# Performance work log

Hardware: AMD Instinct MI355X
Metric: run time of the kernel (lower is better)

## Reference

```python
import jax, jax.numpy as jnp
import numpy as np

BOUNDARY_THRESHOLD = 0.5
TARGET_N = 6.0          # target_avg_token_length
RATIO_LOSS_WEIGHT = 0.03
LR_DIFF = 0.75          # learning_rate_difference
EPS = 1e-8              # torch cosine_similarity eps


def setup_inputs() -> dict:
    key = jax.random.key(0)
    k1, k2, k3 = jax.random.split(key, 3)
    B, L, D, DK = 8, 4096, 1024, 1024
    tokens = jax.random.normal(k1, (B, L, D), dtype=jnp.float32)
    W_qk = jax.random.normal(k2, (D, 2 * DK), dtype=jnp.float32) / np.sqrt(D).astype(np.float32)
    start_key = jax.random.normal(k3, (DK,), dtype=jnp.float32) * 0.01
    return {"tokens": tokens, "W_qk": W_qk, "start_key": start_key}


def _forward(tokens, W_qk, start_key):
    B, L, D = tokens.shape
    qk = tokens @ W_qk                                   # [B, L, 2*Dk]
    queries, keys = jnp.split(qk, 2, axis=-1)
    # keys shifted right by one, with learned start key prepended
    keys_for_sim = jnp.concatenate(
        [jnp.broadcast_to(start_key, (B, 1, keys.shape[-1])), keys[:, :-1]], axis=1)
    qn = jnp.maximum(jnp.linalg.norm(queries, axis=-1), EPS)
    kn = jnp.maximum(jnp.linalg.norm(keys_for_sim, axis=-1), EPS)
    cosine_sim = jnp.sum(queries * keys_for_sim, axis=-1) / (qn * kn)   # [B, L]
    probs = (1.0 - cosine_sim) * 0.5

    boundary_mask = probs > BOUNDARY_THRESHOLD
    boundary_mask = boundary_mask.at[:, 0].set(True)     # first step: first token is boundary
    num_chunks = jnp.sum(boundary_mask, axis=-1)         # [B]

    ar = jnp.arange(L)
    valid = ar[None, :] < num_chunks[:, None]            # [B, L] mask of valid (non-pad) chunks

    # chunk_lens via sorted boundary positions with end sentinel (pads -> length 0)
    bm_end = jnp.concatenate([boundary_mask, jnp.ones((B, 1), dtype=bool)], axis=1)  # [B, L+1]
    pos = jnp.sort(jnp.where(bm_end, jnp.arange(L + 1)[None, :], L + 1), axis=-1)
    chunk_lens = jnp.where(valid, pos[:, 1:] - pos[:, :-1], 0)          # [B, L]

    # compact boundary tokens / probs to the front (pad_sequence equivalent, padded to L)
    bpos = jnp.sort(jnp.where(boundary_mask, ar[None, :], L), axis=-1)  # [B, L]
    safe = jnp.minimum(bpos, L - 1)
    boundary_tokens = jnp.where(valid[..., None],
                                jnp.take_along_axis(tokens, safe[..., None], axis=1), 0.0)
    boundary_probs = jnp.where(valid, jnp.take_along_axis(probs, safe, axis=1), 0.0)
    downsampled = boundary_tokens * boundary_probs[..., None]

    # aux ratio loss (straight-through soft fraction)
    F_hard = boundary_mask.astype(probs.dtype)
    F_soft = jax.nn.sigmoid(probs - BOUNDARY_THRESHOLD)
    F = F_soft + jax.lax.stop_gradient(F_hard - F_soft)
    G = jnp.mean(probs, axis=-1)
    Fm = jnp.mean(F, axis=-1)
    N = TARGET_N
    aux_ratio_loss = N / (N - 1.0) * ((N - 1.0) * Fm * G + (1.0 - Fm) * (1.0 - G))
    weighted_aux_loss = jnp.mean(aux_ratio_loss) * RATIO_LOSS_WEIGHT

    # frac_gradient with frac = 1 / learning_rate_difference (identity fwd, scaled grad)
    frac = 1.0 / LR_DIFF
    ds_scaled = downsampled * frac
    downsampled = ds_scaled + jax.lax.stop_gradient(downsampled - ds_scaled)

    return downsampled, chunk_lens, weighted_aux_loss


def reference(tokens, W_qk, start_key):
    return _forward(tokens, W_qk, start_key)
```

## Files before the change

kernel.cpp:

```cpp
#include <hip/hip_runtime.h>
#include <hip/hip_bf16.h>
#include <hip/hip_fp16.h>


#define B_ 8
#define L_ 4096
#define D_ 1024
#define M_TOT (B_ * L_)
#define BM 128
#define DS_ELEMS ((size_t)M_TOT * D_)
#define SUS_CAP 2048

typedef _Float16 f16x8 __attribute__((ext_vector_type(8)));
typedef _Float16 f16x4 __attribute__((ext_vector_type(4)));
typedef __bf16  bf16x8 __attribute__((ext_vector_type(8)));
typedef __bf16  bf16x4 __attribute__((ext_vector_type(4)));
typedef float   f32x4  __attribute__((ext_vector_type(4)));

typedef __attribute__((address_space(1))) void gv_t;
typedef __attribute__((address_space(3))) void lv_t;

__device__ __forceinline__ void gl_lds16(const void* g, void* l) {
    __builtin_amdgcn_global_load_lds((gv_t*)g, (lv_t*)l, 16, 0, 0);
}

__global__ __launch_bounds__(256)
void prep(const float* __restrict__ tokens, const float* __restrict__ W,
          _Float16* __restrict__ t_h, _Float16* __restrict__ wT_h,
          __bf16* __restrict__ wT_hi, __bf16* __restrict__ wT_lo,
          float* __restrict__ zbase, float* __restrict__ aux_out)
{
    const int bid = blockIdx.x, tid = threadIdx.x;
    if (bid < 8192) {
        const size_t base = (size_t)bid * 4096 + tid * 4;
        #pragma unroll
        for (int r = 0; r < 4; ++r) {
            size_t idx = base + (size_t)r * 1024;
            float4 v = *(const float4*)&tokens[idx];
            f16x4 h;
            h[0] = (_Float16)v.x; h[1] = (_Float16)v.y;
            h[2] = (_Float16)v.z; h[3] = (_Float16)v.w;
            *(f16x4*)&t_h[idx] = h;
        }
    } else if (bid < 10240) {
        __shared__ float lw[32 * 33];
        const int local = bid - 8192;
        const int k0 = (local & 31) * 32;
        const int n0 = (local >> 5) * 32;
        {
            const int lk = tid >> 3, ln4 = (tid & 7) * 4;
            float4 v = *(const float4*)&W[(size_t)(k0 + lk) * 2048 + n0 + ln4];
            lw[(ln4 + 0) * 33 + lk] = v.x;
            lw[(ln4 + 1) * 33 + lk] = v.y;
            lw[(ln4 + 2) * 33 + lk] = v.z;
            lw[(ln4 + 3) * 33 + lk] = v.w;
        }
        __syncthreads();
        {
            const int ln = tid >> 3, lk4 = (tid & 7) * 4;
            f16x4 h; bf16x4 bh, bl;
            #pragma unroll
            for (int j = 0; j < 4; ++j) {
                float v = lw[ln * 33 + lk4 + j];
                h[j] = (_Float16)v;
                __bf16 b = (__bf16)v;
                bh[j] = b;
                bl[j] = (__bf16)(v - (float)b);
            }
            size_t o = (size_t)(n0 + ln) * 1024 + k0 + lk4;
            *(f16x4*)&wT_h[o]   = h;
            *(bf16x4*)&wT_hi[o] = bh;
            *(bf16x4*)&wT_lo[o] = bl;
        }
    } else {
        const int zb = bid - 10240;
        const int i = zb * 1024 + tid * 4;
        if (i < 98308)
            *(float4*)&zbase[i] = make_float4(0.f, 0.f, 0.f, 0.f);
        if (zb == 0 && tid == 0) *aux_out = 0.f;
    }
}

__global__ __launch_bounds__(512, 2)
void gemm_cos_f16(const _Float16* __restrict__ t_h, const _Float16* __restrict__ wT_h,
                  float* __restrict__ dotw, float* __restrict__ qn2w,
                  float* __restrict__ ksn2w,
                  float* __restrict__ qrow, float* __restrict__ krow)
{
    __shared__ float smem[33280];
    float* Ck = smem;

    const int bx = blockIdx.x;
    const int tile_n = (bx >> 3) & 7;
    const int tile_m = ((bx >> 6) & 15) + ((bx & 7) << 4);
    const int m0 = tile_m * 256;
    const int n0 = tile_n * 128;
    const int tid  = threadIdx.x;
    const int w    = tid >> 6;
    const int lane = tid & 63;
    const int quad = lane >> 4;
    const int lc   = lane & 15;

    const int wm  = (w & 3) * 64;
    const int wq0 = (w >> 2) * 64;

    const int st_ch = ((lane & 3) ^ ((lane >> 3) & 3)) * 8;
    const int ia0 = w * 2, ia1 = w * 2 + 1;
    const size_t a_g0 = (size_t)(m0 + ia0 * 16 + (lane >> 2)) * 1024 + st_ch;
    const size_t a_g1 = a_g0 + (size_t)16 * 1024;
    size_t b_g[2];
    #pragma unroll
    for (int j = 0; j < 2; ++j) {
        const int br = (w * 2 + j) * 16 + (lane >> 2);
        const int gr = (br < 128) ? (n0 + br) : (896 + n0 + br);
        b_g[j] = (size_t)gr * 1024 + st_ch;
    }

    char* const sb  = (char*)smem;
    char* const sbB = sb + 49152;
    const int fr_ch = (quad ^ ((lc >> 1) & 3)) * 8;

    f32x4 accq[4][4] = {};
    f32x4 acck[4][4] = {};

#define STAGE_A(KK, BASE)                                                    \
    {                                                                        \
        const size_t kb = (size_t)(KK) * 32;                                 \
        gl_lds16(t_h + a_g0 + kb, (BASE) + ia0 * 1024);                      \
        gl_lds16(t_h + a_g1 + kb, (BASE) + ia1 * 1024);                      \
    }
#define STAGE_B(KK, BASE)                                                    \
    {                                                                        \
        const size_t kb = (size_t)(KK) * 32;                                 \
        gl_lds16(wT_h + b_g[0] + kb, (BASE) + (w * 2 + 0) * 1024);           \
        gl_lds16(wT_h + b_g[1] + kb, (BASE) + (w * 2 + 1) * 1024);           \
    }

    STAGE_A(0, sb)
    STAGE_B(0, sbB)
    STAGE_A(1, sb + 16384)

    int acur = 0;
    int apre = 2;
    for (int kk = 0; kk < 32; ++kk) {
        if (kk < 31) {
            asm volatile("s_waitcnt vmcnt(2)" ::: "memory");
        } else {
            asm volatile("s_waitcnt vmcnt(0)" ::: "memory");
        }
        __builtin_amdgcn_s_barrier();
        if (kk < 31) STAGE_B(kk + 1, sbB + ((kk + 1) & 1) * 16384)
        if (kk < 30) STAGE_A(kk + 2, sb + apre * 16384)

        const _Float16* As = (const _Float16*)(sb + acur * 16384);
        const _Float16* Bs = (const _Float16*)(sbB + (kk & 1) * 16384);

        f16x8 af[4], bq[4], bk[4];
        #pragma unroll
        for (int mi = 0; mi < 4; ++mi)
            af[mi] = *(const f16x8*)(As + (wm + mi * 16 + lc) * 32 + fr_ch);
        #pragma unroll
        for (int ni = 0; ni < 4; ++ni) {
            bq[ni] = *(const f16x8*)(Bs + (wq0 + ni * 16 + lc) * 32 + fr_ch);
            bk[ni] = *(const f16x8*)(Bs + (128 + wq0 + ni * 16 + lc) * 32 + fr_ch);
        }
        #pragma unroll
        for (int mi = 0; mi < 4; ++mi) {
            #pragma unroll
            for (int ni = 0; ni < 4; ++ni) {
                accq[mi][ni] = __builtin_amdgcn_mfma_f32_16x16x32_f16(
                    af[mi], bq[ni], accq[mi][ni], 0, 0, 0);
                acck[mi][ni] = __builtin_amdgcn_mfma_f32_16x16x32_f16(
                    af[mi], bk[ni], acck[mi][ni], 0, 0, 0);
            }
        }
        acur = (acur == 2) ? 0 : acur + 1;
        apre = (apre == 2) ? 0 : apre + 1;
    }
#undef STAGE_A
#undef STAGE_B
    __syncthreads();

    #pragma unroll
    for (int mi = 0; mi < 4; ++mi) {
        #pragma unroll
        for (int reg = 0; reg < 4; ++reg) {
            const int row = wm + mi * 16 + quad * 4 + reg;
            float s = 0.f, s2 = 0.f;
            #pragma unroll
            for (int ni = 0; ni < 4; ++ni) {
                s  += accq[mi][ni][reg] * accq[mi][ni][reg];
                s2 += acck[mi][ni][reg] * acck[mi][ni][reg];
            }
            s += __shfl_xor(s, 1); s += __shfl_xor(s, 2);
            s += __shfl_xor(s, 4); s += __shfl_xor(s, 8);
            if (lc == 0) atomicAdd(&qn2w[m0 + row], s);

            s2 += __shfl_xor(s2, 1); s2 += __shfl_xor(s2, 2);
            s2 += __shfl_xor(s2, 4); s2 += __shfl_xor(s2, 8);
            if (lc == 0 && row < 255) atomicAdd(&ksn2w[m0 + row + 1], s2);
        }
    }

    #pragma unroll
    for (int mi = 0; mi < 4; ++mi)
        #pragma unroll
        for (int ni = 0; ni < 4; ++ni)
            #pragma unroll
            for (int reg = 0; reg < 4; ++reg)
                Ck[(wm + mi * 16 + quad * 4 + reg) * 130 + wq0 + ni * 16 + lc] =
                    acck[mi][ni][reg];
    __syncthreads();

    #pragma unroll
    for (int mi = 0; mi < 4; ++mi) {
        #pragma unroll
        for (int reg = 0; reg < 4; ++reg) {
            const int row = wm + mi * 16 + quad * 4 + reg;
            float d = 0.f;
            if (row >= 1) {
                #pragma unroll
                for (int ni = 0; ni < 4; ++ni)
                    d += accq[mi][ni][reg]
                       * Ck[(row - 1) * 130 + wq0 + ni * 16 + lc];
            }
            d += __shfl_xor(d, 1); d += __shfl_xor(d, 2);
            d += __shfl_xor(d, 4); d += __shfl_xor(d, 8);
            if (lc == 0 && row >= 1) atomicAdd(&dotw[m0 + row], d);
        }
    }

    if (wm == 0 && quad == 0) {
        #pragma unroll
        for (int ni = 0; ni < 4; ++ni)
            qrow[(size_t)(tile_m * 2) * D_ + n0 + wq0 + ni * 16 + lc] =
                accq[0][ni][0];
    }
    if (wm == 128 && quad == 0) {
        #pragma unroll
        for (int ni = 0; ni < 4; ++ni)
            qrow[(size_t)(tile_m * 2 + 1) * D_ + n0 + wq0 + ni * 16 + lc] =
                accq[0][ni][0];
    }
    if (wm == 64 && quad == 3) {
        #pragma unroll
        for (int ni = 0; ni < 4; ++ni)
            krow[(size_t)(tile_m * 2) * D_ + n0 + wq0 + ni * 16 + lc] =
                acck[3][ni][3];
    }
    if (wm == 192 && quad == 3) {
        #pragma unroll
        for (int ni = 0; ni < 4; ++ni)
            krow[(size_t)(tile_m * 2 + 1) * D_ + n0 + wq0 + ni * 16 + lc] =
                acck[3][ni][3];
    }
}

__global__ __launch_bounds__(256)
void probs_fused(const float* __restrict__ qrow, const float* __restrict__ krow,
                 const float* __restrict__ start_key,
                 const float* __restrict__ dotw, const float* __restrict__ qn2w,
                 const float* __restrict__ ksn2w, float* __restrict__ probsw,
                 int* __restrict__ scount, int* __restrict__ slist)
{
    const int tile = blockIdx.x;
    const int tid = threadIdx.x;
    __shared__ float sd[4], sk[4];

    {
        const float* q  = qrow + (size_t)tile * D_;
        const float* ks = ((tile & 31) == 0) ? start_key
                                             : (krow + (size_t)(tile - 1) * D_);
        float4 qv = *(const float4*)&q[tid * 4];
        float4 kv = *(const float4*)&ks[tid * 4];
        float d  = qv.x * kv.x + qv.y * kv.y + qv.z * kv.z + qv.w * kv.w;
        float k2 = kv.x * kv.x + kv.y * kv.y + kv.z * kv.z + kv.w * kv.w;
        #pragma unroll
        for (int off = 32; off; off >>= 1) {
            d  += __shfl_down(d, off, 64);
            k2 += __shfl_down(k2, off, 64);
        }
        const int lane = tid & 63, wid = tid >> 6;
        if (lane == 0) { sd[wid] = d; sk[wid] = k2; }
    }
    __syncthreads();

    if (tid < BM) {
        const int m = tile * BM + tid;
        float dd = dotw[m], kk = ksn2w[m];
        if (tid == 0) {
            dd = sd[0] + sd[1] + sd[2] + sd[3];
            kk = sk[0] + sk[1] + sk[2] + sk[3];
        }
        float qn = fmaxf(sqrtf(qn2w[m]), 1e-8f);
        float kn = fmaxf(sqrtf(kk), 1e-8f);
        float c = dd / (qn * kn);
        probsw[m] = 0.5f * (1.f - c);
        if (fabsf(c) < 1e-3f) {
            int i = atomicAdd(scount, 1);
            if (i < SUS_CAP) slist[i] = m;
        }
    }
}

__global__ __launch_bounds__(256)
void gather_split(const float* __restrict__ tokens, const int* __restrict__ scount,
                  const int* __restrict__ slist,
                  __bf16* __restrict__ As_hi, __bf16* __restrict__ As_lo)
{
    int n = *scount; if (n > SUS_CAP) n = SUS_CAP;
    const int n_up = (n + 127) & ~127;
    const int slot = blockIdx.x;
    const int sl = slot & 2047;
    if (sl >= n_up) return;
    const int tid = threadIdx.x;

    int src = -1;
    if (sl < n) {
        int t = slist[sl];
        if (slot < 2048) src = t;
        else src = ((t & 4095) == 0) ? t : (t - 1);
    }
    bf16x4 h = {}, l = {};
    if (src >= 0) {
        float4 v = *(const float4*)&tokens[(size_t)src * 1024 + tid * 4];
        float vs[4] = {v.x, v.y, v.z, v.w};
        #pragma unroll
        for (int j = 0; j < 4; ++j) {
            __bf16 b = (__bf16)vs[j];
            h[j] = b;
            l[j] = (__bf16)(vs[j] - (float)b);
        }
    }
    size_t o = (size_t)slot * 1024 + tid * 4;
    *(bf16x4*)&As_hi[o] = h;
    *(bf16x4*)&As_lo[o] = l;
}

__global__ __launch_bounds__(256, 2)
void gemm2(const __bf16* __restrict__ As_hi, const __bf16* __restrict__ As_lo,
           const __bf16* __restrict__ wT_hi, const __bf16* __restrict__ wT_lo,
           const int* __restrict__ scount, float* __restrict__ C2)
{
    int n = *scount; if (n > SUS_CAP) n = SUS_CAP;
    const int tm = blockIdx.y;
    const int local_base = (tm < 16) ? tm * 128 : (tm - 16) * 128;
    if (local_base >= n) return;
    const int m0 = (tm < 16) ? tm * 128 : 2048 + (tm - 16) * 128;

    __shared__ float smem[12288];

    const int tile_n = blockIdx.x;
    const int n0 = tile_n * 128;
    const int colbase = ((tm < 16) ? 0 : 1024) + n0;
    const int tid  = threadIdx.x;
    const int w    = tid >> 6;
    const int lane = tid & 63;
    const int quad = lane >> 4;
    const int lc   = lane & 15;
    const int wm  = (w & 1) * 64;
    const int wq0 = (w >> 1) * 32;

    const int ia0 = w * 2, ia1 = w * 2 + 1;
    const int st_ch = ((lane & 3) ^ ((lane >> 3) & 3)) * 8;
    const size_t a_g0 = (size_t)(m0 + ia0 * 16 + (lane >> 2)) * 1024 + st_ch;
    const size_t a_g1 = a_g0 + (size_t)16 * 1024;
    const int br0 = ia0 * 16 + (lane >> 2);
    const int br1 = br0 + 16;
    const size_t b_g0 = (size_t)(colbase + br0) * 1024 + st_ch;
    const size_t b_g1 = (size_t)(colbase + br1) * 1024 + st_ch;

    char* const sb = (char*)smem;
    const int fr_ch = (quad ^ ((lc >> 1) & 3)) * 8;

    f32x4 accq[4][2] = {};
    f32x4 acck[4][2] = {};

    gl_lds16(As_hi + a_g0,      sb + ia0 * 1024);
    gl_lds16(As_hi + a_g1,      sb + ia1 * 1024);
    gl_lds16(wT_hi + b_g0,      sb + 8192 + ia0 * 1024);
    gl_lds16(wT_hi + b_g1,      sb + 8192 + ia1 * 1024);
    gl_lds16(As_hi + a_g0 + 32, sb + 16384 + ia0 * 1024);
    gl_lds16(As_hi + a_g1 + 32, sb + 16384 + ia1 * 1024);
    gl_lds16(wT_hi + b_g0 + 32, sb + 16384 + 8192 + ia0 * 1024);
    gl_lds16(wT_hi + b_g1 + 32, sb + 16384 + 8192 + ia1 * 1024);

    int cur = 0;
    for (int kk = 0; kk < 96; ++kk) {
        if (kk < 95) {
            asm volatile("s_waitcnt vmcnt(4)" ::: "memory");
        } else {
            asm volatile("s_waitcnt vmcnt(0)" ::: "memory");
        }
        __builtin_amdgcn_s_barrier();
        if (kk < 94) {
            const int k2 = kk + 2;
            const int slab2 = k2 >> 5;
            const size_t kb2 = (size_t)(k2 & 31) * 32;
            const __bf16* Ap2 = (slab2 < 2) ? As_hi : As_lo;
            const __bf16* Bp2 = (slab2 == 1) ? wT_lo : wT_hi;
            int nxt = cur + 2; if (nxt >= 3) nxt -= 3;
            char* nb = sb + nxt * 16384;
            gl_lds16(Ap2 + a_g0 + kb2, nb + ia0 * 1024);
            gl_lds16(Ap2 + a_g1 + kb2, nb + ia1 * 1024);
            gl_lds16(Bp2 + b_g0 + kb2, nb + 8192 + ia0 * 1024);
            gl_lds16(Bp2 + b_g1 + kb2, nb + 8192 + ia1 * 1024);
        }
        const __bf16* As = (const __bf16*)(sb + cur * 16384);
        const __bf16* Bs = As + 4096;

        bf16x8 af[4], bq[2], bk[2];
        #pragma unroll
        for (int mi = 0; mi < 4; ++mi)
            af[mi] = *(const bf16x8*)(As + (wm + mi * 16 + lc) * 32 + fr_ch);
        #pragma unroll
        for (int ni = 0; ni < 2; ++ni) {
            bq[ni] = *(const bf16x8*)(Bs + (wq0 + ni * 16 + lc) * 32 + fr_ch);
            bk[ni] = *(const bf16x8*)(Bs + (64 + wq0 + ni * 16 + lc) * 32 + fr_ch);
        }
        #pragma unroll
        for (int mi = 0; mi < 4; ++mi) {
            #pragma unroll
            for (int ni = 0; ni < 2; ++ni) {
                accq[mi][ni] = __builtin_amdgcn_mfma_f32_16x16x32_bf16(
                    af[mi], bq[ni], accq[mi][ni], 0, 0, 0);
                acck[mi][ni] = __builtin_amdgcn_mfma_f32_16x16x32_bf16(
                    af[mi], bk[ni], acck[mi][ni], 0, 0, 0);
            }
        }
        cur = (cur == 2) ? 0 : cur + 1;
    }

    #pragma unroll
    for (int mi = 0; mi < 4; ++mi) {
        #pragma unroll
        for (int reg = 0; reg < 4; ++reg) {
            const int row = m0 + wm + mi * 16 + quad * 4 + reg;
            #pragma unroll
            for (int ni = 0; ni < 2; ++ni) {
                C2[(size_t)row * 2048 + colbase + wq0 + ni * 16 + lc] = accq[mi][ni][reg];
                C2[(size_t)row * 2048 + colbase + 64 + wq0 + ni * 16 + lc] = acck[mi][ni][reg];
            }
        }
    }
}

__global__ __launch_bounds__(256)
void dot_fix(const float* __restrict__ C2, const float* __restrict__ start_key,
             const int* __restrict__ scount, const int* __restrict__ slist,
             float* __restrict__ probsw, int* __restrict__ scount2,
             int* __restrict__ slist2, float* __restrict__ fix3acc)
{
    int n = *scount; if (n > SUS_CAP) n = SUS_CAP;
    const int s = blockIdx.x;
    if (s >= n) return;
    const int tid = threadIdx.x;
    const int t = slist[s];
    const bool st = (t & 4095) == 0;
    const float* q = C2 + (size_t)s * 2048;
    const float* k = st ? start_key : (C2 + (size_t)(2048 + s) * 2048 + 1024);

    float4 qv = *(const float4*)&q[tid * 4];
    float4 kv = *(const float4*)&k[tid * 4];
    float d  = qv.x * kv.x + qv.y * kv.y + qv.z * kv.z + qv.w * kv.w;
    float q2 = qv.x * qv.x + qv.y * qv.y + qv.z * qv.z + qv.w * qv.w;
    float k2 = kv.x * kv.x + kv.y * kv.y + kv.z * kv.z + kv.w * kv.w;
    #pragma unroll
    for (int off = 32; off; off >>= 1) {
        d  += __shfl_down(d, off, 64);
        q2 += __shfl_down(q2, off, 64);
        k2 += __shfl_down(k2, off, 64);
    }
    __shared__ float sd[4], sq[4], sk[4];
    const int lane = tid & 63, wid = tid >> 6;
    if (lane == 0) { sd[wid] = d; sq[wid] = q2; sk[wid] = k2; }
    __syncthreads();
    if (tid == 0) {
        float D  = sd[0] + sd[1] + sd[2] + sd[3];
        float Q2 = sq[0] + sq[1] + sq[2] + sq[3];
        float K2 = sk[0] + sk[1] + sk[2] + sk[3];
        float c = D / (fmaxf(sqrtf(Q2), 1e-8f) * fmaxf(sqrtf(K2), 1e-8f));
        if (fabsf(c) < 1e-4f) {
            int i = atomicAdd(scount2, 1);
            if (i < SUS_CAP) {
                slist2[i] = t;
                float* fa = fix3acc + 3 * i;
                fa[0] = 0.f; fa[1] = 0.f; fa[2] = 0.f;
            }
        } else {
            probsw[t] = 0.5f * (1.f - c);
        }
    }
}

__global__ __launch_bounds__(256)
void fixup3a(const float* __restrict__ tokens, const float* __restrict__ W,
             const float* __restrict__ start_key, const int* __restrict__ scount2,
             const int* __restrict__ slist2, float* __restrict__ fix3acc)
{
    __shared__ float ta[1024], tb[1024], kvs[128];
    const int tid = threadIdx.x;
    const int lane = tid & 63;
    const int c = blockIdx.x & 7;
    int n = *scount2; if (n > SUS_CAP) n = SUS_CAP;

    for (int i = blockIdx.x >> 3; i < n; i += 128) {
        const int t = slist2[i];
        const bool st = (t & 4095) == 0;
        *(float4*)&ta[tid * 4] = *(const float4*)&tokens[(size_t)t * 1024 + tid * 4];
        if (!st)
            *(float4*)&tb[tid * 4] = *(const float4*)&tokens[(size_t)(t - 1) * 1024 + tid * 4];
        __syncthreads();

        float qd = 0.f, q2p = 0.f, k2p = 0.f, dotp = 0.f;
        if (tid < 128) {
            const float* Wp = W + c * 128 + tid;
            float a0 = 0.f, a1 = 0.f, a2 = 0.f, a3 = 0.f;
            for (int k = 0; k < 1024; k += 4) {
                a0 = fmaf(ta[k + 0], Wp[(size_t)(k + 0) * 2048], a0);
                a1 = fmaf(ta[k + 1], Wp[(size_t)(k + 1) * 2048], a1);
                a2 = fmaf(ta[k + 2], Wp[(size_t)(k + 2) * 2048], a2);
                a3 = fmaf(ta[k + 3], Wp[(size_t)(k + 3) * 2048], a3);
            }
            qd = (a0 + a1) + (a2 + a3);
            q2p = qd * qd;
        } else {
            const int j = tid - 128;
            float kd;
            if (st) {
                kd = start_key[c * 128 + j];
            } else {
                const float* Wp = W + 1024 + c * 128 + j;
                float a0 = 0.f, a1 = 0.f, a2 = 0.f, a3 = 0.f;
                for (int k = 0; k < 1024; k += 4) {
                    a0 = fmaf(tb[k + 0], Wp[(size_t)(k + 0) * 2048], a0);
                    a1 = fmaf(tb[k + 1], Wp[(size_t)(k + 1) * 2048], a1);
                    a2 = fmaf(tb[k + 2], Wp[(size_t)(k + 2) * 2048], a2);
                    a3 = fmaf(tb[k + 3], Wp[(size_t)(k + 3) * 2048], a3);
                }
                kd = (a0 + a1) + (a2 + a3);
            }
            kvs[j] = kd;
            k2p = kd * kd;
        }
        __syncthreads();
        if (tid < 128) dotp = qd * kvs[tid];

        #pragma unroll
        for (int off = 32; off; off >>= 1) {
            dotp += __shfl_down(dotp, off, 64);
            q2p  += __shfl_down(q2p,  off, 64);
            k2p  += __shfl_down(k2p,  off, 64);
        }
        if (lane == 0) {
            float* fa = fix3acc + 3 * i;
            atomicAdd(&fa[0], dotp);
            atomicAdd(&fa[1], q2p);
            atomicAdd(&fa[2], k2p);
        }
        __syncthreads();
    }
}

__global__ __launch_bounds__(256)
void fixup3b(const int* __restrict__ scount2, const int* __restrict__ slist2,
             const float* __restrict__ fix3acc, float* __restrict__ probsw)
{
    int n = *scount2; if (n > SUS_CAP) n = SUS_CAP;
    for (int i = threadIdx.x + blockIdx.x * 256; i < n; i += 256 * gridDim.x) {
        const int t = slist2[i];
        const float* fa = fix3acc + 3 * i;
        float D = fa[0], Q2 = fa[1], K2 = fa[2];
        float qn = fmaxf(sqrtf(Q2), 1e-8f), kn = fmaxf(sqrtf(K2), 1e-8f);
        probsw[t] = 0.5f * (1.f - D / (qn * kn));
    }
}

__global__ __launch_bounds__(1024)
void chunk_scan_p(const float* __restrict__ probsw, int* __restrict__ bposw,
                  int* __restrict__ ncw, float* __restrict__ aux_out,
                  float* __restrict__ out_lens)
{
    const int b = blockIdx.x, tid = threadIdx.x;
    const int lane = tid & 63, wid = tid >> 6;
    __shared__ int wcnt[16];
    __shared__ float wsum[16];
    __shared__ int s_nc;
    __shared__ float s_ps;

    const int base = b * L_ + tid * 4;
    float4 pv = *(const float4*)&probsw[base];
    const float p[4] = {pv.x, pv.y, pv.z, pv.w};

    bool mk[4]; int cnt = 0; float psum = 0.f;
    #pragma unroll
    for (int j = 0; j < 4; ++j) {
        mk[j] = (p[j] > 0.5f) || ((tid * 4 + j) == 0);
        cnt += mk[j] ? 1 : 0;
        psum += p[j];
    }
    int inc = cnt;
    #pragma unroll
    for (int off = 1; off < 64; off <<= 1) {
        int nn = __shfl_up(inc, off, 64);
        if (lane >= off) inc += nn;
    }
    float ps = psum;
    #pragma unroll
    for (int off = 32; off; off >>= 1) ps += __shfl_down(ps, off, 64);
    if (lane == 63) wcnt[wid] = inc;
    if (lane == 0)  wsum[wid] = ps;
    __syncthreads();
    if (tid == 0) {
        int run = 0; float tt = 0.f;
        for (int i = 0; i < 16; ++i) { int c = wcnt[i]; wcnt[i] = run; run += c; tt += wsum[i]; }
        s_nc = run; s_ps = tt;
    }
    __syncthreads();
    const int nc = s_nc;
    int idx = wcnt[wid] + (inc - cnt);
    #pragma unroll
    for (int j = 0; j < 4; ++j)
        if (mk[j]) { bposw[b * L_ + idx] = tid * 4 + j; ++idx; }
    if (tid == 0) {
        ncw[b] = nc;
        float G  = s_ps * (1.f / L_);
        float Fm = (float)nc * (1.f / L_);
        atomicAdd(aux_out, 0.0045f * (5.f * Fm * G + (1.f - Fm) * (1.f - G)));
    }
    __syncthreads();
    #pragma unroll
    for (int j = 0; j < 4; ++j) {
        int i = tid * 4 + j;
        float len = 0.f;
        if (i < nc) {
            int pi  = bposw[b * L_ + i];
            int nxt = (i + 1 < nc) ? bposw[b * L_ + i + 1] : L_;
            len = (float)(nxt - pi);
        }
        out_lens[b * L_ + i] = len;
    }
}

__global__ __launch_bounds__(256)
void gather_ds(const float* __restrict__ tokens, const float* __restrict__ probsw,
               const int* __restrict__ bposw, const int* __restrict__ ncw,
               float* __restrict__ out)
{
    const int row = blockIdx.x;
    const int b = row >> 12, i = row & 4095;
    const int nc = ncw[b];
    float4 v = make_float4(0.f, 0.f, 0.f, 0.f);
    if (i < nc) {
        const int t = bposw[b * L_ + i];
        const float pv = probsw[b * L_ + t];
        float4 tv = *(const float4*)&tokens[((size_t)(b << 12) + t) * D_ + threadIdx.x * 4];
        v = make_float4(tv.x * pv, tv.y * pv, tv.z * pv, tv.w * pv);
    }
    *(float4*)&out[(size_t)row * D_ + threadIdx.x * 4] = v;
}

extern "C" void kernel_launch(void* const* d_in, const int* in_sizes, int n_in,
                              void* d_out, int out_size, void* d_ws, size_t ws_size,
                              hipStream_t stream)
{
    const float* tokens    = (const float*)d_in[0];
    const float* W_qk      = (const float*)d_in[1];
    const float* start_key = (const float*)d_in[2];
    float* out = (float*)d_out;
    float* lens_out = out + DS_ELEMS;
    float* aux_out  = out + DS_ELEMS + M_TOT;

    float* wf = (float*)d_ws;
    float* dotw    = wf;
    float* qn2w    = wf + 32768;
    float* ksn2w   = wf + 65536;
    int*   scount  = (int*)(wf + 98304);
    int*   scount2 = (int*)(wf + 98305);
    float* probsw  = wf + 98308;
    int*   bposw   = (int*)(wf + 131076);
    int*   ncw     = (int*)(wf + 163844);
    int*   slist   = (int*)(wf + 163852);
    int*   slist2  = (int*)(wf + 165900);
    float* qrow    = wf + 167948;
    float* krow    = wf + 430092;
    _Float16* wT_h = (_Float16*)(wf + 692236);

    _Float16* t_h  = (_Float16*)out;
    __bf16* As_hi  = (__bf16*)(out + 16777216);
    __bf16* As_lo  = (__bf16*)(out + 18874368);
    float*  C2     = out + 20971520;
    __bf16* wT_hi  = (__bf16*)(out + 29360128);
    __bf16* wT_lo  = (__bf16*)(out + 30408704);
    float* fix3acc = out + 18874368;

    prep<<<10337, 256, 0, stream>>>(tokens, W_qk, t_h, wT_h, wT_hi, wT_lo,
                                    wf, aux_out);
    gemm_cos_f16<<<1024, 512, 0, stream>>>(t_h, wT_h, dotw, qn2w, ksn2w,
                                           qrow, krow);
    probs_fused<<<256, 256, 0, stream>>>(qrow, krow, start_key, dotw, qn2w,
                                         ksn2w, probsw, scount, slist);
    gather_split<<<4096, 256, 0, stream>>>(tokens, scount, slist, As_hi, As_lo);
    gemm2<<<dim3(8, 32), 256, 0, stream>>>(As_hi, As_lo, wT_hi, wT_lo,
                                           scount, C2);
    dot_fix<<<2048, 256, 0, stream>>>(C2, start_key, scount, slist, probsw,
                                      scount2, slist2, fix3acc);
    fixup3a<<<1024, 256, 0, stream>>>(tokens, W_qk, start_key, scount2, slist2,
                                      fix3acc);
    fixup3b<<<8, 256, 0, stream>>>(scount2, slist2, fix3acc, probsw);
    chunk_scan_p<<<B_, 1024, 0, stream>>>(probsw, bposw, ncw, aux_out, lens_out);
    gather_ds<<<M_TOT, 256, 0, stream>>>(tokens, probsw, bposw, ncw, out);
}
```

Baseline: 550.6 us.

## Split gemm2 K-loop across three hi/lo slabs and sum partials in dot_fix

The refinement GEMM for suspicious rows previously ran all three bf16 hi/lo product slabs serially in one 96-step K loop per block. Each slab now runs in its own block along grid z, writing separate partial outputs into scratch regions of the output buffer. dot_fix sums the three partials before the dot products. This triples parallelism for a small, occupancy-starved grid, at the cost of extra partial writes and reads. fixup3b's grid also grows from 8 to 32 blocks.

```diff
diff --git a/kernel.cpp b/kernel.cpp
--- a/kernel.cpp
+++ b/kernel.cpp
@@ -10,6 +10,10 @@
 #define BM 128
 #define DS_ELEMS ((size_t)M_TOT * D_)
 #define SUS_CAP 2048
+
+#define C2A_OFF 20971520u
+#define C2B_OFF 0u
+#define C2C_OFF 8388608u
 
 typedef _Float16 f16x8 __attribute__((ext_vector_type(8)));
 typedef _Float16 f16x4 __attribute__((ext_vector_type(4)));
@@ -340,13 +344,18 @@
 __global__ __launch_bounds__(256, 2)
 void gemm2(const __bf16* __restrict__ As_hi, const __bf16* __restrict__ As_lo,
            const __bf16* __restrict__ wT_hi, const __bf16* __restrict__ wT_lo,
-           const int* __restrict__ scount, float* __restrict__ C2)
+           const int* __restrict__ scount, float* __restrict__ outb)
 {
     int n = *scount; if (n > SUS_CAP) n = SUS_CAP;
     const int tm = blockIdx.y;
     const int local_base = (tm < 16) ? tm * 128 : (tm - 16) * 128;
     if (local_base >= n) return;
     const int m0 = (tm < 16) ? tm * 128 : 2048 + (tm - 16) * 128;
+
+    const int slab = blockIdx.z;
+    const __bf16* Ap = (slab == 2) ? As_lo : As_hi;
+    const __bf16* Bp = (slab == 1) ? wT_lo : wT_hi;
+    float* C2 = outb + ((slab == 0) ? C2A_OFF : (slab == 1) ? C2B_OFF : C2C_OFF);
 
     __shared__ float smem[12288];
 
@@ -376,35 +385,31 @@
     f32x4 accq[4][2] = {};
     f32x4 acck[4][2] = {};
 
-    gl_lds16(As_hi + a_g0,      sb + ia0 * 1024);
-    gl_lds16(As_hi + a_g1,      sb + ia1 * 1024);
-    gl_lds16(wT_hi + b_g0,      sb + 8192 + ia0 * 1024);
-    gl_lds16(wT_hi + b_g1,      sb + 8192 + ia1 * 1024);
-    gl_lds16(As_hi + a_g0 + 32, sb + 16384 + ia0 * 1024);
-    gl_lds16(As_hi + a_g1 + 32, sb + 16384 + ia1 * 1024);
-    gl_lds16(wT_hi + b_g0 + 32, sb + 16384 + 8192 + ia0 * 1024);
-    gl_lds16(wT_hi + b_g1 + 32, sb + 16384 + 8192 + ia1 * 1024);
+    gl_lds16(Ap + a_g0,      sb + ia0 * 1024);
+    gl_lds16(Ap + a_g1,      sb + ia1 * 1024);
+    gl_lds16(Bp + b_g0,      sb + 8192 + ia0 * 1024);
+    gl_lds16(Bp + b_g1,      sb + 8192 + ia1 * 1024);
+    gl_lds16(Ap + a_g0 + 32, sb + 16384 + ia0 * 1024);
+    gl_lds16(Ap + a_g1 + 32, sb + 16384 + ia1 * 1024);
+    gl_lds16(Bp + b_g0 + 32, sb + 16384 + 8192 + ia0 * 1024);
+    gl_lds16(Bp + b_g1 + 32, sb + 16384 + 8192 + ia1 * 1024);
 
     int cur = 0;
-    for (int kk = 0; kk < 96; ++kk) {
-        if (kk < 95) {
+    for (int kk = 0; kk < 32; ++kk) {
+        if (kk < 31) {
             asm volatile("s_waitcnt vmcnt(4)" ::: "memory");
         } else {
             asm volatile("s_waitcnt vmcnt(0)" ::: "memory");
         }
         __builtin_amdgcn_s_barrier();
-        if (kk < 94) {
-            const int k2 = kk + 2;
-            const int slab2 = k2 >> 5;
-            const size_t kb2 = (size_t)(k2 & 31) * 32;
-            const __bf16* Ap2 = (slab2 < 2) ? As_hi : As_lo;
-            const __bf16* Bp2 = (slab2 == 1) ? wT_lo : wT_hi;
+        if (kk < 30) {
+            const size_t kb2 = (size_t)(kk + 2) * 32;
             int nxt = cur + 2; if (nxt >= 3) nxt -= 3;
             char* nb = sb + nxt * 16384;
-            gl_lds16(Ap2 + a_g0 + kb2, nb + ia0 * 1024);
-            gl_lds16(Ap2 + a_g1 + kb2, nb + ia1 * 1024);
-            gl_lds16(Bp2 + b_g0 + kb2, nb + 8192 + ia0 * 1024);
-            gl_lds16(Bp2 + b_g1 + kb2, nb + 8192 + ia1 * 1024);
+            gl_lds16(Ap + a_g0 + kb2, nb + ia0 * 1024);
+            gl_lds16(Ap + a_g1 + kb2, nb + ia1 * 1024);
+            gl_lds16(Bp + b_g0 + kb2, nb + 8192 + ia0 * 1024);
+            gl_lds16(Bp + b_g1 + kb2, nb + 8192 + ia1 * 1024);
         }
         const __bf16* As = (const __bf16*)(sb + cur * 16384);
         const __bf16* Bs = As + 4096;
@@ -446,7 +451,7 @@
 }
 
 __global__ __launch_bounds__(256)
-void dot_fix(const float* __restrict__ C2, const float* __restrict__ start_key,
+void dot_fix(const float* __restrict__ outb, const float* __restrict__ start_key,
              const int* __restrict__ scount, const int* __restrict__ slist,
              float* __restrict__ probsw, int* __restrict__ scount2,
              int* __restrict__ slist2, float* __restrict__ fix3acc)
@@ -457,11 +462,24 @@
     const int tid = threadIdx.x;
     const int t = slist[s];
     const bool st = (t & 4095) == 0;
-    const float* q = C2 + (size_t)s * 2048;
-    const float* k = st ? start_key : (C2 + (size_t)(2048 + s) * 2048 + 1024);
-
-    float4 qv = *(const float4*)&q[tid * 4];
-    float4 kv = *(const float4*)&k[tid * 4];
+    const size_t qoff = (size_t)s * 2048 + tid * 4;
+    const size_t koff = (size_t)(2048 + s) * 2048 + 1024 + tid * 4;
+
+    float4 qa = *(const float4*)&outb[C2A_OFF + qoff];
+    float4 qb = *(const float4*)&outb[C2B_OFF + qoff];
+    float4 qc = *(const float4*)&outb[C2C_OFF + qoff];
+    float4 qv = make_float4(qa.x + qb.x + qc.x, qa.y + qb.y + qc.y,
+                            qa.z + qb.z + qc.z, qa.w + qb.w + qc.w);
+    float4 kv;
+    if (st) {
+        kv = *(const float4*)&start_key[tid * 4];
+    } else {
+        float4 ka = *(const float4*)&outb[C2A_OFF + koff];
+        float4 kb = *(const float4*)&outb[C2B_OFF + koff];
+        float4 kc = *(const float4*)&outb[C2C_OFF + koff];
+        kv = make_float4(ka.x + kb.x + kc.x, ka.y + kb.y + kc.y,
+                         ka.z + kb.z + kc.z, ka.w + kb.w + kc.w);
+    }
     float d  = qv.x * kv.x + qv.y * kv.y + qv.z * kv.z + qv.w * kv.w;
     float q2 = qv.x * qv.x + qv.y * qv.y + qv.z * qv.z + qv.w * qv.w;
     float k2 = kv.x * kv.x + kv.y * kv.y + kv.z * kv.z + kv.w * kv.w;
@@ -689,7 +707,6 @@
     _Float16* t_h  = (_Float16*)out;
     __bf16* As_hi  = (__bf16*)(out + 16777216);
     __bf16* As_lo  = (__bf16*)(out + 18874368);
-    float*  C2     = out + 20971520;
     __bf16* wT_hi  = (__bf16*)(out + 29360128);
     __bf16* wT_lo  = (__bf16*)(out + 30408704);
     float* fix3acc = out + 18874368;
@@ -701,13 +718,13 @@
     probs_fused<<<256, 256, 0, stream>>>(qrow, krow, start_key, dotw, qn2w,
                                          ksn2w, probsw, scount, slist);
     gather_split<<<4096, 256, 0, stream>>>(tokens, scount, slist, As_hi, As_lo);
-    gemm2<<<dim3(8, 32), 256, 0, stream>>>(As_hi, As_lo, wT_hi, wT_lo,
-                                           scount, C2);
-    dot_fix<<<2048, 256, 0, stream>>>(C2, start_key, scount, slist, probsw,
+    gemm2<<<dim3(8, 32, 3), 256, 0, stream>>>(As_hi, As_lo, wT_hi, wT_lo,
+                                              scount, out);
+    dot_fix<<<2048, 256, 0, stream>>>(out, start_key, scount, slist, probsw,
                                       scount2, slist2, fix3acc);
     fixup3a<<<1024, 256, 0, stream>>>(tokens, W_qk, start_key, scount2, slist2,
                                       fix3acc);
-    fixup3b<<<8, 256, 0, stream>>>(scount2, slist2, fix3acc, probsw);
+    fixup3b<<<32, 256, 0, stream>>>(scount2, slist2, fix3acc, probsw);
     chunk_scan_p<<<B_, 1024, 0, stream>>>(probsw, bposw, ncw, aux_out, lens_out);
     gather_ds<<<M_TOT, 256, 0, stream>>>(tokens, probsw, bposw, ncw, out);
 }
```

After: 546.5 us. About the same (-0.7%).
